# Kernel optimization log

Measured on AMD Instinct MI355X. Metric: run time of the kernel, lower is better.

## Reference

```python
import jax, jax.numpy as jnp
import numpy as np

EPS = 1e-5

def setup_inputs() -> dict:
    key = jax.random.key(0)
    ks = jax.random.split(key, 10)
    B, C, H, W = 4, 512, 56, 56
    n_heads = 8
    nq = H * W
    oq = (H // 2) * (W // 2)  # sr_ratio=2, k=3,s=2,p=1 -> halved spatial dims
    s = 0.02
    return {
        'x': jax.random.normal(ks[0], (B, C, H, W), jnp.float32),
        'attn_weights': jax.random.uniform(ks[1], (B, n_heads, nq, oq), jnp.float32),
        'q_w': jax.random.normal(ks[2], (C, C), jnp.float32) * s,
        'k_w': jax.random.normal(ks[3], (C, C), jnp.float32) * s,
        'v_w': jax.random.normal(ks[4], (C, C), jnp.float32) * s,
        'sr_w': jax.random.normal(ks[5], (C, 1, 3, 3), jnp.float32) * s,  # depthwise OIHW
        'sr_b': jnp.zeros((C,), jnp.float32),
        'ln_g': jnp.ones((C,), jnp.float32),
        'ln_b': jnp.zeros((C,), jnp.float32),
        'tc_w': jax.random.normal(ks[6], (n_heads, n_heads), jnp.float32) * 0.3,  # 1x1 conv over heads
        'tc_b': jnp.zeros((n_heads,), jnp.float32),
        'proj_w': jax.random.normal(ks[7], (C, C), jnp.float32) * s,
        'proj_b': jnp.zeros((C,), jnp.float32),
    }

def _layernorm(x, g, b):
    m = jnp.mean(x, axis=-1, keepdims=True)
    v = jnp.var(x, axis=-1, keepdims=True)
    return (x - m) * jax.lax.rsqrt(v + EPS) * g + b

def reference(x, attn_weights, q_w, k_w, v_w, sr_w, sr_b, ln_g, ln_b, tc_w, tc_b, proj_w, proj_b):
    B, C, H, W = x.shape
    n_heads = tc_w.shape[0]
    hd = C // n_heads
    scale = hd ** -0.5
    nq = H * W
    xf = x.reshape(B, C, nq).transpose(0, 2, 1)  # (B, nq, C)
    q = (xf @ q_w.T).reshape(B, nq, n_heads, hd).transpose(0, 2, 1, 3)  # (B, h, nq, hd)
    # spatial reduction: depthwise conv k=3, s=2, p=1 on NCHW, then LayerNorm
    xs = jax.lax.conv_general_dilated(
        x, sr_w, window_strides=(2, 2), padding=((1, 1), (1, 1)),
        feature_group_count=C, dimension_numbers=('NCHW', 'OIHW', 'NCHW'))
    xs = xs + sr_b[None, :, None, None]
    oq = xs.shape[2] * xs.shape[3]
    xs = xs.reshape(B, C, oq).transpose(0, 2, 1)  # (B, oq, C)
    xs = _layernorm(xs, ln_g, ln_b)
    k = (xs @ k_w.T).reshape(B, oq, n_heads, hd).transpose(0, 2, 3, 1)  # (B, h, hd, oq)
    v = (xs @ v_w.T).reshape(B, oq, n_heads, hd).transpose(0, 2, 1, 3)  # (B, h, oq, hd)
    attn = jnp.einsum('bhqd,bhdo->bhqo', q, k) * scale  # (B, h, nq, oq)
    # apply_transform: 1x1 conv mixing heads -> softmax -> InstanceNorm2d (no affine)
    attn = jnp.einsum('bhqo,gh->bgqo', attn, tc_w) + tc_b[None, :, None, None]
    attn = jax.nn.softmax(attn, axis=-1)
    m = jnp.mean(attn, axis=(2, 3), keepdims=True)
    var = jnp.var(attn, axis=(2, 3), keepdims=True)
    attn = (attn - m) * jax.lax.rsqrt(var + EPS)
    attn = attn_weights * attn
    out = jnp.einsum('bhqo,bhod->bhqd', attn, v)  # (B, h, nq, hd)
    out = out.transpose(0, 2, 1, 3).reshape(B, nq, C)
    out = out @ proj_w.T + proj_b
    return out.reshape(B, H, W, C).transpose(0, 3, 1, 2)
```

## Files before the change

### kernel.cpp

```cpp
#include <hip/hip_runtime.h>

typedef _Float16 half8 __attribute__((ext_vector_type(8)));
typedef _Float16 half4 __attribute__((ext_vector_type(4)));
typedef float fx4 __attribute__((ext_vector_type(4)));

#define MFMA16(a,b,c) __builtin_amdgcn_mfma_f32_16x16x32_f16(a,b,c,0,0,0)

#define BN 4
#define CC 512
#define HH 56
#define WW 56
#define NQ 3136
#define OQ 784
#define NH 8
#define HD 64
#define NSEG 7
#define BGN (BN * NH * NQ)

__device__ inline half8 h8z() {
    half8 v;
#pragma unroll
    for (int j = 0; j < 8; j++) v[j] = (_Float16)0.f;
    return v;
}

__global__ void cvt4_kernel(const float* __restrict__ a, const float* __restrict__ b,
                            const float* __restrict__ c, const float* __restrict__ d,
                            _Float16* __restrict__ o, float* __restrict__ S2) {
    if (blockIdx.x == 0 && blockIdx.y == 0 && threadIdx.x < 32) S2[threadIdx.x] = 0.f;
    int y = blockIdx.y;
    const float* s = (y == 0) ? a : (y == 1) ? b : (y == 2) ? c : d;
    int i = blockIdx.x * 256 + threadIdx.x;
    o[(size_t)y * 262144 + i] = (_Float16)s[i];
}

__global__ void xpose_kernel(const float* __restrict__ x, _Float16* __restrict__ xf) {
    __shared__ float t[32][33];
    int n0 = blockIdx.x * 32, c0 = blockIdx.y * 32, b = blockIdx.z;
    int tx = threadIdx.x, ty = threadIdx.y;
#pragma unroll
    for (int i = 0; i < 4; i++)
        t[ty + 8 * i][tx] = x[((size_t)(b * CC) + c0 + ty + 8 * i) * NQ + n0 + tx];
    __syncthreads();
#pragma unroll
    for (int i = 0; i < 4; i++)
        xf[((size_t)(b * NQ) + n0 + ty + 8 * i) * CC + c0 + tx] = (_Float16)t[tx][ty + 8 * i];
}

__global__ void dw_kernel(const float* __restrict__ x, const float* __restrict__ w,
                          const float* __restrict__ bias, float* __restrict__ xsc) {
    int cb = blockIdx.x, oy = blockIdx.y, b = blockIdx.z;
    int tx = threadIdx.x, ty = threadIdx.y;
    int c = cb * 16 + ty;
    float a = bias[c];
    const float* xp = x + ((size_t)(b * CC + c) * HH) * WW;
#pragma unroll
    for (int ky = 0; ky < 3; ky++) {
        int iy = 2 * oy - 1 + ky;
        if (iy < 0 || iy >= HH) continue;
#pragma unroll
        for (int kx = 0; kx < 3; kx++) {
            int ix = 2 * tx - 1 + kx;
            if (ix < 0 || ix >= WW) continue;
            a += xp[iy * WW + ix] * w[c * 9 + ky * 3 + kx];
        }
    }
    __shared__ float tile[28][17];
    tile[tx][ty] = a;
    __syncthreads();
    int lin = ty * 28 + tx;
    int oi = lin >> 4, ci = lin & 15;
    xsc[((size_t)(b * OQ) + oy * 28 + oi) * CC + cb * 16 + ci] = tile[oi][ci];
}

__global__ __launch_bounds__(256) void ln_kernel(const float* __restrict__ xsc,
        const float* __restrict__ g, const float* __restrict__ bb,
        _Float16* __restrict__ xs16) {
    int row = blockIdx.x;
    const float* rp = xsc + (size_t)row * CC;
    int t = threadIdx.x;
    float v0 = rp[t], v1 = rp[t + 256];
    float s = v0 + v1, ss = v0 * v0 + v1 * v1;
#pragma unroll
    for (int m = 1; m < 64; m <<= 1) {
        s += __shfl_xor(s, m, 64);
        ss += __shfl_xor(ss, m, 64);
    }
    __shared__ float red[8];
    int wv = t >> 6;
    if ((t & 63) == 0) { red[wv] = s; red[4 + wv] = ss; }
    __syncthreads();
    s = red[0] + red[1] + red[2] + red[3];
    ss = red[4] + red[5] + red[6] + red[7];
    float mean = s * (1.f / 512.f);
    float var = ss * (1.f / 512.f) - mean * mean;
    float rs = rsqrtf(var + 1e-5f);
    xs16[(size_t)row * CC + t] = (_Float16)((v0 - mean) * rs * g[t] + bb[t]);
    xs16[(size_t)row * CC + t + 256] = (_Float16)((v1 - mean) * rs * g[t + 256] + bb[t + 256]);
}

__global__ __launch_bounds__(256) void gemm_qkv(const _Float16* __restrict__ xf,
        const _Float16* __restrict__ xs, const _Float16* __restrict__ w4,
        _Float16* __restrict__ q16, _Float16* __restrict__ k16, _Float16* __restrict__ vT) {
    const int which = blockIdx.z;
    if (which && blockIdx.x >= 49) return;
    const _Float16* A = which ? xs : xf;
    const _Float16* Bw = w4 + (size_t)which * 262144;
    __shared__ _Float16 As[64 * 72];
    __shared__ _Float16 Bs[64 * 72];
    const int m0 = blockIdx.x * 64, n0 = blockIdx.y * 64;
    const int tid = threadIdx.x;
    const int lane = tid & 63, wv = tid >> 6;
    const int wm = (wv >> 1) * 32, wn = (wv & 1) * 32;
    const int l15 = lane & 15, quad = lane >> 4;
    fx4 acc[2][2];
#pragma unroll
    for (int i = 0; i < 2; i++)
#pragma unroll
        for (int j = 0; j < 2; j++) acc[i][j] = fx4{0.f, 0.f, 0.f, 0.f};
    for (int k0 = 0; k0 < 512; k0 += 64) {
        __syncthreads();
#pragma unroll
        for (int i = 0; i < 2; i++) {
            int id = tid + 256 * i;
            int r = id >> 3, kc = (id & 7) << 3;
            *(half8*)(As + r * 72 + kc) = *(const half8*)(A + (size_t)(m0 + r) * 512 + k0 + kc);
            *(half8*)(Bs + r * 72 + kc) = *(const half8*)(Bw + (size_t)(n0 + r) * 512 + k0 + kc);
        }
        __syncthreads();
#pragma unroll
        for (int ks = 0; ks < 2; ks++) {
            half8 af[2], bf[2];
#pragma unroll
            for (int s = 0; s < 2; s++) {
                af[s] = *(const half8*)(As + (wm + s * 16 + l15) * 72 + ks * 32 + quad * 8);
                bf[s] = *(const half8*)(Bs + (wn + s * 16 + l15) * 72 + ks * 32 + quad * 8);
            }
#pragma unroll
            for (int i = 0; i < 2; i++)
#pragma unroll
                for (int j = 0; j < 2; j++)
                    acc[i][j] = MFMA16(af[i], bf[j], acc[i][j]);
        }
    }
    if (which < 2) {
        _Float16* O = which ? k16 : q16;
#pragma unroll
        for (int i = 0; i < 2; i++)
#pragma unroll
            for (int j = 0; j < 2; j++) {
                int col = n0 + wn + j * 16 + l15;
#pragma unroll
                for (int e = 0; e < 4; e++) {
                    int row = m0 + wm + i * 16 + quad * 4 + e;
                    O[(size_t)row * 512 + col] = (_Float16)acc[i][j][e];
                }
            }
    } else {
#pragma unroll
        for (int i = 0; i < 2; i++) {
            int row = m0 + wm + i * 16 + quad * 4;
            int b = row / OQ;
            int o = row - b * OQ;
#pragma unroll
            for (int j = 0; j < 2; j++) {
                int c = n0 + wn + j * 16 + l15;
                half4 pk;
#pragma unroll
                for (int e = 0; e < 4; e++) pk[e] = (_Float16)acc[i][j][e];
                *(half4*)(vT + ((size_t)(b * NH + (c >> 6)) * HD + (c & 63)) * OQ + o) = pk;
            }
        }
    }
}

__global__ __launch_bounds__(256) void qk_mix(const _Float16* __restrict__ q16,
        const _Float16* __restrict__ k16, const float* __restrict__ tcw,
        const float* __restrict__ tcb, _Float16* __restrict__ L,
        float* __restrict__ Zpart, float* __restrict__ E2part) {
    __shared__ _Float16 kl[16 * 520];
    __shared__ float tcs[64];
    __shared__ float tbb[8];
    const int b = blockIdx.z, oseg = blockIdx.y, ob = oseg * 112;
    const int tid = threadIdx.x;
    const int wv = tid >> 6, lane = tid & 63, l15 = lane & 15, quad = lane >> 4;
    const int n0 = blockIdx.x * 64 + wv * 16;
    if (tid < 64) tcs[tid] = tcw[tid] * 0.125f;
    else if (tid < 72) tbb[tid - 64] = tcb[tid - 64];

    half8 aF[8][2];
    const _Float16* qrow = q16 + ((size_t)(b * NQ + n0 + l15)) * 512;
#pragma unroll
    for (int h = 0; h < 8; h++)
#pragma unroll
        for (int ks = 0; ks < 2; ks++)
            aF[h][ks] = *(const half8*)(qrow + h * 64 + ks * 32 + quad * 8);

    float z[8][4], s2[8][4];
#pragma unroll
    for (int g = 0; g < 8; g++)
#pragma unroll
        for (int e = 0; e < 4; e++) { z[g][e] = 0.f; s2[g][e] = 0.f; }

    for (int ot = 0; ot < 7; ot++) {
        int o0 = ob + ot * 16;
        __syncthreads();
        const _Float16* kb = k16 + ((size_t)(b * OQ + o0)) * 512;
#pragma unroll
        for (int i = 0; i < 4; i++) {
            int id = tid + 256 * i;
            int r = id >> 6, c = (id & 63) << 3;
            *(half8*)(kl + r * 520 + c) = *(const half8*)(kb + (size_t)r * 512 + c);
        }
        __syncthreads();
        fx4 s[8];
#pragma unroll
        for (int h = 0; h < 8; h++) {
            fx4 a = fx4{0.f, 0.f, 0.f, 0.f};
#pragma unroll
            for (int ks = 0; ks < 2; ks++) {
                half8 bF = *(const half8*)(kl + l15 * 520 + h * 64 + ks * 32 + quad * 8);
                a = MFMA16(aF[h][ks], bF, a);
            }
            s[h] = a;
        }
#pragma unroll
        for (int g = 0; g < 8; g++) {
            size_t tb = (((size_t)(b * 8 + g) * 196 + (n0 >> 4)) * 49 + (o0 >> 4)) * 256
                        + (l15 >> 3) * 128 + (l15 & 7);
#pragma unroll
            for (int e = 0; e < 4; e++) {
                float v = tbb[g];
#pragma unroll
                for (int h = 0; h < 8; h++) v += tcs[g * 8 + h] * s[h][e];
                _Float16 vh = (_Float16)v;
                float vr = (float)vh;
                float ex = __expf(vr);
                z[g][e] += ex;
                s2[g][e] += ex * ex;
                L[tb + (quad * 4 + e) * 8] = vh;
            }
        }
    }
#pragma unroll
    for (int m = 1; m < 16; m <<= 1) {
#pragma unroll
        for (int g = 0; g < 8; g++)
#pragma unroll
            for (int e = 0; e < 4; e++) {
                z[g][e] += __shfl_xor(z[g][e], m, 64);
                s2[g][e] += __shfl_xor(s2[g][e], m, 64);
            }
    }
    if (l15 < 8) {
        int g = l15;
        size_t base = (size_t)oseg * BGN + (size_t)(b * 8 + g) * NQ + n0 + quad * 4;
#pragma unroll
        for (int e = 0; e < 4; e++) {
            Zpart[base + e] = z[g][e];
            E2part[base + e] = s2[g][e];
        }
    }
}

__global__ __launch_bounds__(256) void zfin_kernel(const float* __restrict__ Zpart,
        const float* __restrict__ E2part, float* __restrict__ Zinv, float* __restrict__ S2) {
    int i = blockIdx.x * 256 + threadIdx.x;
    float z = 0.f, e2 = 0.f;
#pragma unroll
    for (int s = 0; s < NSEG; s++) {
        z += Zpart[(size_t)s * BGN + i];
        e2 += E2part[(size_t)s * BGN + i];
    }
    float zi = 1.f / z;
    Zinv[i] = zi;
    float r = e2 * zi * zi;
#pragma unroll
    for (int m = 1; m < 64; m <<= 1) r += __shfl_xor(r, m, 64);
    if ((threadIdx.x & 63) == 0) atomicAdd(&S2[i / NQ], r);
}

__global__ __launch_bounds__(256) void pv_kernel(const _Float16* __restrict__ Lt,
        const float* __restrict__ W, const _Float16* __restrict__ vT,
        const float* __restrict__ Zinv, const float* __restrict__ S2,
        _Float16* __restrict__ outp) {
    __shared__ float Ws[4][2][16 * 70];
    const int b = blockIdx.z, g = blockIdx.y;
    const int tid = threadIdx.x;
    const int wv = tid >> 6, lane = tid & 63, l15 = lane & 15, quad = lane >> 4;
    const int n0 = blockIdx.x * 64 + wv * 16;
    const int bg = b * 8 + g;
    const float mm = 1.f / (float)OQ;
    const float rv = rsqrtf(S2[bg] * (1.f / ((float)NQ * (float)OQ)) - mm * mm + 1e-5f);
    const float czr = Zinv[bg * NQ + n0 + l15] * rv;
    const float rm = rv * mm;
    const _Float16* Lb = Lt + (((size_t)bg * 196 + (n0 >> 4)) * 49) * 256 + lane * 8;
    const float* Wg = W + ((size_t)bg * NQ + n0 + (lane >> 4)) * OQ + (lane & 15) * 4;
    const float* Wrow = W + ((size_t)bg * NQ + n0 + l15) * OQ;
    const _Float16* vb = vT + (size_t)bg * HD * OQ + (size_t)l15 * OQ;
    float* WsW = &Ws[wv][0][0];
    const float* WsR = &Ws[wv][0][0] + l15 * 70 + quad * 8;

    fx4 wreg[4];
    half8 lA, lB, vA0, vA1, vA2, vA3, vB0, vB1, vB2, vB3;
    fx4 acc0 = fx4{0.f, 0.f, 0.f, 0.f};
    fx4 acc1 = fx4{0.f, 0.f, 0.f, 0.f};
    fx4 acc2 = fx4{0.f, 0.f, 0.f, 0.f};
    fx4 acc3 = fx4{0.f, 0.f, 0.f, 0.f};

#define LOADWG(g2)                                                           \
    {                                                                        \
        _Pragma("unroll") for (int i = 0; i < 4; i++)                        \
            wreg[i] = *(const fx4*)(Wg + (size_t)(4 * i) * OQ + (g2) * 64);  \
    }
#define DSWR(ph)                                                             \
    {                                                                        \
        _Pragma("unroll") for (int i = 0; i < 4; i++)                        \
            *(fx4*)(WsW + (ph) * (16 * 70) + ((lane >> 4) + 4 * i) * 70 +    \
                    (lane & 15) * 4) = wreg[i];                              \
    }
#define LOADL(c, d)                                                          \
    {                                                                        \
        if ((c) < 24 || lane < 32) d = *(const half8*)(Lb + (c) * 512);      \
        else d = h8z();                                                      \
    }
#define LOADV(c, d0, d1, d2, d3)                                             \
    {                                                                        \
        int kb = (c) * 32 + quad * 8;                                        \
        if (kb < OQ) {                                                       \
            d0 = *(const half8*)(vb + (size_t)(0 * 16) * OQ + kb);           \
            d1 = *(const half8*)(vb + (size_t)(1 * 16) * OQ + kb);           \
            d2 = *(const half8*)(vb + (size_t)(2 * 16) * OQ + kb);           \
            d3 = *(const half8*)(vb + (size_t)(3 * 16) * OQ + kb);           \
        } else { d0 = h8z(); d1 = h8z(); d2 = h8z(); d3 = h8z(); }           \
    }
#define COMPUTE_W(sL, wf0, wf1, s0, s1, s2, s3)                              \
    {                                                                        \
        half8 aH;                                                            \
        _Pragma("unroll") for (int j = 0; j < 8; j++) {                      \
            float e = __expf((float)sL[j]);                                  \
            float a = e * czr - rm;                                          \
            float wx = (j < 4) ? wf0[j] : wf1[j - 4];                        \
            aH[j] = (_Float16)(a * wx);                                      \
        }                                                                    \
        acc0 = MFMA16(aH, s0, acc0);                                         \
        acc1 = MFMA16(aH, s1, acc1);                                         \
        acc2 = MFMA16(aH, s2, acc2);                                         \
        acc3 = MFMA16(aH, s3, acc3);                                         \
    }

    LOADWG(0);
    LOADL(0, lA);
    LOADV(0, vA0, vA1, vA2, vA3);
    DSWR(0);
    LOADWG(1);

#pragma unroll 1
    for (int pi = 0; pi < 12; ++pi) {
        const int phC = pi & 1, phN = phC ^ 1;
        if (pi <= 10) DSWR(phN);
        if (pi <= 9) LOADWG(pi + 2);
        const int c0 = 2 * pi;
        LOADL(c0 + 1, lB);
        LOADV(c0 + 1, vB0, vB1, vB2, vB3);
        {
            const float* wr = WsR + phC * (16 * 70);
            fx4 wf0 = *(const fx4*)(wr);
            fx4 wf1 = *(const fx4*)(wr + 4);
            COMPUTE_W(lA, wf0, wf1, vA0, vA1, vA2, vA3);
        }
        LOADL(c0 + 2, lA);
        LOADV(c0 + 2, vA0, vA1, vA2, vA3);
        {
            const float* wr = WsR + phC * (16 * 70) + 32;
            fx4 wf0 = *(const fx4*)(wr);
            fx4 wf1 = *(const fx4*)(wr + 4);
            COMPUTE_W(lB, wf0, wf1, vB0, vB1, vB2, vB3);
        }
    }
    {
        fx4 wt0 = fx4{0.f, 0.f, 0.f, 0.f};
        fx4 wt1 = fx4{0.f, 0.f, 0.f, 0.f};
        int kb = 768 + quad * 8;
        if (kb < OQ) {
            wt0 = *(const fx4*)(Wrow + kb);
            wt1 = *(const fx4*)(Wrow + kb + 4);
        }
        COMPUTE_W(lA, wt0, wt1, vA0, vA1, vA2, vA3);
    }
#undef LOADWG
#undef DSWR
#undef LOADL
#undef LOADV
#undef COMPUTE_W

    fx4 acc[4] = {acc0, acc1, acc2, acc3};
#pragma unroll
    for (int ds = 0; ds < 4; ds++)
#pragma unroll
        for (int e = 0; e < 4; e++) {
            int n = n0 + quad * 4 + e;
            int c = g * 64 + ds * 16 + l15;
            outp[((size_t)b * NQ + n) * 512 + c] = (_Float16)acc[ds][e];
        }
}

__global__ __launch_bounds__(256) void gemm_proj(const _Float16* __restrict__ A,
        const _Float16* __restrict__ Ball, const float* __restrict__ bias,
        float* __restrict__ Oall) {
    __shared__ _Float16 As[64 * 72];
    __shared__ _Float16 Bs[64 * 72];
    const int b = blockIdx.z;
    const _Float16* Bm = Ball + (size_t)b * NQ * 512;
    float* O = Oall + (size_t)b * CC * NQ;
    const int m0 = blockIdx.x * 64, n0 = blockIdx.y * 64;
    const int tid = threadIdx.x;
    const int lane = tid & 63, wv = tid >> 6;
    const int wm = (wv >> 1) * 32, wn = (wv & 1) * 32;
    const int l15 = lane & 15, quad = lane >> 4;
    fx4 acc[2][2];
#pragma unroll
    for (int i = 0; i < 2; i++)
#pragma unroll
        for (int j = 0; j < 2; j++) acc[i][j] = fx4{0.f, 0.f, 0.f, 0.f};
    for (int k0 = 0; k0 < 512; k0 += 64) {
        __syncthreads();
#pragma unroll
        for (int i = 0; i < 2; i++) {
            int id = tid + 256 * i;
            int r = id >> 3, kc = (id & 7) << 3;
            *(half8*)(As + r * 72 + kc) = *(const half8*)(A + (size_t)(m0 + r) * 512 + k0 + kc);
            *(half8*)(Bs + r * 72 + kc) = *(const half8*)(Bm + (size_t)(n0 + r) * 512 + k0 + kc);
        }
        __syncthreads();
#pragma unroll
        for (int ks = 0; ks < 2; ks++) {
            half8 af[2], bf[2];
#pragma unroll
            for (int s = 0; s < 2; s++) {
                af[s] = *(const half8*)(As + (wm + s * 16 + l15) * 72 + ks * 32 + quad * 8);
                bf[s] = *(const half8*)(Bs + (wn + s * 16 + l15) * 72 + ks * 32 + quad * 8);
            }
#pragma unroll
            for (int i = 0; i < 2; i++)
#pragma unroll
                for (int j = 0; j < 2; j++)
                    acc[i][j] = MFMA16(af[i], bf[j], acc[i][j]);
        }
    }
#pragma unroll
    for (int i = 0; i < 2; i++)
#pragma unroll
        for (int j = 0; j < 2; j++) {
            int col = n0 + wn + j * 16 + l15;
#pragma unroll
            for (int e = 0; e < 4; e++) {
                int row = m0 + wm + i * 16 + quad * 4 + e;
                O[(size_t)row * NQ + col] = acc[i][j][e] + bias[row];
            }
        }
}

extern "C" void kernel_launch(void* const* d_in, const int* in_sizes, int n_in,
                              void* d_out, int out_size, void* d_ws, size_t ws_size,
                              hipStream_t stream) {
    const float* x = (const float*)d_in[0];
    const float* aw = (const float*)d_in[1];
    const float* q_w = (const float*)d_in[2];
    const float* k_w = (const float*)d_in[3];
    const float* v_w = (const float*)d_in[4];
    const float* sr_w = (const float*)d_in[5];
    const float* sr_b = (const float*)d_in[6];
    const float* ln_g = (const float*)d_in[7];
    const float* ln_b = (const float*)d_in[8];
    const float* tc_w = (const float*)d_in[9];
    const float* tc_b = (const float*)d_in[10];
    const float* p_w = (const float*)d_in[11];
    const float* p_b = (const float*)d_in[12];
    float* out = (float*)d_out;

    char* p = (char*)d_ws;
    auto take = [&](size_t bytes) -> char* {
        char* r = p;
        p += (bytes + 255) & ~(size_t)255;
        return r;
    };
    _Float16* qw16 = (_Float16*)take(512 * 512 * 2);
    _Float16* kw16 = (_Float16*)take(512 * 512 * 2);
    _Float16* vw16 = (_Float16*)take(512 * 512 * 2);
    _Float16* pw16 = (_Float16*)take(512 * 512 * 2);
    _Float16* xf16 = (_Float16*)take((size_t)BN * NQ * CC * 2);
    float* xsc = (float*)take((size_t)BN * OQ * CC * 4);
    _Float16* xs16 = (_Float16*)take((size_t)BN * OQ * CC * 2);
    _Float16* q16 = (_Float16*)take((size_t)BN * NQ * CC * 2);
    _Float16* k16 = (_Float16*)take((size_t)BN * OQ * CC * 2);
    _Float16* vT = (_Float16*)take((size_t)BN * OQ * CC * 2);
    _Float16* outp = (_Float16*)take((size_t)BN * NQ * CC * 2);
    float* Zpart = (float*)take((size_t)NSEG * BGN * 4);
    float* E2part = (float*)take((size_t)NSEG * BGN * 4);
    float* S2 = (float*)take(32 * 4);
    float* Zinv = (float*)take((size_t)BGN * 4);
    _Float16* L = (_Float16*)take((size_t)BN * NH * NQ * OQ * 2);

    cvt4_kernel<<<dim3(1024, 4), 256, 0, stream>>>(q_w, k_w, v_w, p_w, qw16, S2);
    xpose_kernel<<<dim3(98, 16, BN), dim3(32, 8), 0, stream>>>(x, xf16);
    dw_kernel<<<dim3(32, 28, BN), dim3(28, 16), 0, stream>>>(x, sr_w, sr_b, xsc);
    ln_kernel<<<BN * OQ, 256, 0, stream>>>(xsc, ln_g, ln_b, xs16);
    gemm_qkv<<<dim3(196, 8, 3), 256, 0, stream>>>(xf16, xs16, qw16, q16, k16, vT);
    qk_mix<<<dim3(49, 7, BN), 256, 0, stream>>>(q16, k16, tc_w, tc_b, L, Zpart, E2part);
    zfin_kernel<<<BGN / 256, 256, 0, stream>>>(Zpart, E2part, Zinv, S2);
    pv_kernel<<<dim3(49, 8, BN), 256, 0, stream>>>(L, aw, vT, Zinv, S2, outp);
    gemm_proj<<<dim3(8, 49, BN), 256, 0, stream>>>(pw16, outp, p_b, out);
}
```

Before: 706.5 us.

## Double-buffer LDS staging via direct global-to-LDS loads with XOR swizzle

The QKV GEMM, the QK/head-mix kernel and the projection GEMM now stage tiles into LDS with global_load_lds 16-byte direct loads instead of register round-trips. Each uses two LDS buffers so the next tile is prefetched while the current one is multiplied, which also drops one barrier per iteration. Padded rows are replaced by an XOR swizzle of 8-element groups to avoid bank conflicts. LDS use doubles, and correctness relies on the compiler waiting for the LDS DMA before the barriers.

```diff
diff --git a/kernel.cpp b/kernel.cpp
--- a/kernel.cpp
+++ b/kernel.cpp
@@ -22,6 +22,12 @@
 #pragma unroll
     for (int j = 0; j < 8; j++) v[j] = (_Float16)0.f;
     return v;
+}
+
+__device__ __forceinline__ void glds16(const void* g, void* l) {
+    __builtin_amdgcn_global_load_lds(
+        (__attribute__((address_space(1))) const unsigned int*)g,
+        (__attribute__((address_space(3))) unsigned int*)l, 16, 0, 0);
 }
 
 __global__ void cvt4_kernel(const float* __restrict__ a, const float* __restrict__ b,
@@ -106,8 +112,8 @@
     if (which && blockIdx.x >= 49) return;
     const _Float16* A = which ? xs : xf;
     const _Float16* Bw = w4 + (size_t)which * 262144;
-    __shared__ _Float16 As[64 * 72];
-    __shared__ _Float16 Bs[64 * 72];
+    __shared__ _Float16 As[2][64 * 64];
+    __shared__ _Float16 Bs[2][64 * 64];
     const int m0 = blockIdx.x * 64, n0 = blockIdx.y * 64;
     const int tid = threadIdx.x;
     const int lane = tid & 63, wv = tid >> 6;
@@ -118,23 +124,34 @@
     for (int i = 0; i < 2; i++)
 #pragma unroll
         for (int j = 0; j < 2; j++) acc[i][j] = fx4{0.f, 0.f, 0.f, 0.f};
-    for (int k0 = 0; k0 < 512; k0 += 64) {
-        __syncthreads();
-#pragma unroll
-        for (int i = 0; i < 2; i++) {
-            int id = tid + 256 * i;
-            int r = id >> 3, kc = (id & 7) << 3;
-            *(half8*)(As + r * 72 + kc) = *(const half8*)(A + (size_t)(m0 + r) * 512 + k0 + kc);
-            *(half8*)(Bs + r * 72 + kc) = *(const half8*)(Bw + (size_t)(n0 + r) * 512 + k0 + kc);
-        }
-        __syncthreads();
+
+#define STAGEG(bf, kk)                                                       \
+    {                                                                        \
+        _Pragma("unroll") for (int i = 0; i < 2; i++) {                      \
+            int id = tid + 256 * i;                                          \
+            int r = id >> 3, gg = id & 7;                                    \
+            int gs = gg ^ (r & 7);                                           \
+            glds16(A + (size_t)(m0 + r) * 512 + (kk) + gs * 8,               \
+                   &As[bf][(id & ~63) * 8]);                                 \
+            glds16(Bw + (size_t)(n0 + r) * 512 + (kk) + gs * 8,              \
+                   &Bs[bf][(id & ~63) * 8]);                                 \
+        }                                                                    \
+    }
+
+    STAGEG(0, 0);
+    __syncthreads();
+    for (int kt = 0; kt < 8; kt++) {
+        const int cur = kt & 1;
+        if (kt < 7) STAGEG(cur ^ 1, (kt + 1) * 64);
 #pragma unroll
         for (int ks = 0; ks < 2; ks++) {
             half8 af[2], bf[2];
 #pragma unroll
             for (int s = 0; s < 2; s++) {
-                af[s] = *(const half8*)(As + (wm + s * 16 + l15) * 72 + ks * 32 + quad * 8);
-                bf[s] = *(const half8*)(Bs + (wn + s * 16 + l15) * 72 + ks * 32 + quad * 8);
+                int ra = wm + s * 16 + l15;
+                int rb = wn + s * 16 + l15;
+                af[s] = *(const half8*)(&As[cur][ra * 64 + ((ks * 4 + quad) ^ (ra & 7)) * 8]);
+                bf[s] = *(const half8*)(&Bs[cur][rb * 64 + ((ks * 4 + quad) ^ (rb & 7)) * 8]);
             }
 #pragma unroll
             for (int i = 0; i < 2; i++)
@@ -142,7 +159,10 @@
                 for (int j = 0; j < 2; j++)
                     acc[i][j] = MFMA16(af[i], bf[j], acc[i][j]);
         }
-    }
+        __syncthreads();
+    }
+#undef STAGEG
+
     if (which < 2) {
         _Float16* O = which ? k16 : q16;
 #pragma unroll
@@ -178,7 +198,7 @@
         const _Float16* __restrict__ k16, const float* __restrict__ tcw,
         const float* __restrict__ tcb, _Float16* __restrict__ L,
         float* __restrict__ Zpart, float* __restrict__ E2part) {
-    __shared__ _Float16 kl[16 * 520];
+    __shared__ _Float16 kl[2][16 * 512];
     __shared__ float tcs[64];
     __shared__ float tbb[8];
     const int b = blockIdx.z, oseg = blockIdx.y, ob = oseg * 112;
@@ -202,24 +222,33 @@
 #pragma unroll
         for (int e = 0; e < 4; e++) { z[g][e] = 0.f; s2[g][e] = 0.f; }
 
+#define STAGEK(bf, oo)                                                       \
+    {                                                                        \
+        const _Float16* kbp = k16 + ((size_t)(b * OQ + (oo))) * 512;         \
+        _Pragma("unroll") for (int i = 0; i < 4; i++) {                      \
+            int id = tid + 256 * i;                                          \
+            int r = id >> 6, g16 = id & 63;                                  \
+            int gs = (g16 & 56) | ((g16 & 7) ^ (r & 7));                     \
+            glds16(kbp + (size_t)r * 512 + gs * 8, &kl[bf][(id & ~63) * 8]); \
+        }                                                                    \
+    }
+
+    STAGEK(0, ob);
+    __syncthreads();
+
     for (int ot = 0; ot < 7; ot++) {
+        const int cur = ot & 1;
+        if (ot < 6) STAGEK(cur ^ 1, ob + (ot + 1) * 16);
         int o0 = ob + ot * 16;
-        __syncthreads();
-        const _Float16* kb = k16 + ((size_t)(b * OQ + o0)) * 512;
-#pragma unroll
-        for (int i = 0; i < 4; i++) {
-            int id = tid + 256 * i;
-            int r = id >> 6, c = (id & 63) << 3;
-            *(half8*)(kl + r * 520 + c) = *(const half8*)(kb + (size_t)r * 512 + c);
-        }
-        __syncthreads();
         fx4 s[8];
 #pragma unroll
         for (int h = 0; h < 8; h++) {
             fx4 a = fx4{0.f, 0.f, 0.f, 0.f};
 #pragma unroll
             for (int ks = 0; ks < 2; ks++) {
-                half8 bF = *(const half8*)(kl + l15 * 520 + h * 64 + ks * 32 + quad * 8);
+                int colg = h * 8 + ks * 4 + quad;
+                int rg = (colg & 56) | ((colg & 7) ^ (l15 & 7));
+                half8 bF = *(const half8*)(&kl[cur][l15 * 512 + rg * 8]);
                 a = MFMA16(aF[h][ks], bF, a);
             }
             s[h] = a;
@@ -241,7 +270,10 @@
                 L[tb + (quad * 4 + e) * 8] = vh;
             }
         }
-    }
+        __syncthreads();
+    }
+#undef STAGEK
+
 #pragma unroll
     for (int m = 1; m < 16; m <<= 1) {
 #pragma unroll
@@ -408,8 +440,8 @@
 __global__ __launch_bounds__(256) void gemm_proj(const _Float16* __restrict__ A,
         const _Float16* __restrict__ Ball, const float* __restrict__ bias,
         float* __restrict__ Oall) {
-    __shared__ _Float16 As[64 * 72];
-    __shared__ _Float16 Bs[64 * 72];
+    __shared__ _Float16 As[2][64 * 64];
+    __shared__ _Float16 Bs[2][64 * 64];
     const int b = blockIdx.z;
     const _Float16* Bm = Ball + (size_t)b * NQ * 512;
     float* O = Oall + (size_t)b * CC * NQ;
@@ -423,23 +455,34 @@
     for (int i = 0; i < 2; i++)
 #pragma unroll
         for (int j = 0; j < 2; j++) acc[i][j] = fx4{0.f, 0.f, 0.f, 0.f};
-    for (int k0 = 0; k0 < 512; k0 += 64) {
-        __syncthreads();
-#pragma unroll
-        for (int i = 0; i < 2; i++) {
-            int id = tid + 256 * i;
-            int r = id >> 3, kc = (id & 7) << 3;
-            *(half8*)(As + r * 72 + kc) = *(const half8*)(A + (size_t)(m0 + r) * 512 + k0 + kc);
-            *(half8*)(Bs + r * 72 + kc) = *(const half8*)(Bm + (size_t)(n0 + r) * 512 + k0 + kc);
-        }
-        __syncthreads();
+
+#define STAGEP(bf, kk)                                                       \
+    {                                                                        \
+        _Pragma("unroll") for (int i = 0; i < 2; i++) {                      \
+            int id = tid + 256 * i;                                          \
+            int r = id >> 3, gg = id & 7;                                    \
+            int gs = gg ^ (r & 7);                                           \
+            glds16(A + (size_t)(m0 + r) * 512 + (kk) + gs * 8,               \
+                   &As[bf][(id & ~63) * 8]);                                 \
+            glds16(Bm + (size_t)(n0 + r) * 512 + (kk) + gs * 8,              \
+                   &Bs[bf][(id & ~63) * 8]);                                 \
+        }                                                                    \
+    }
+
+    STAGEP(0, 0);
+    __syncthreads();
+    for (int kt = 0; kt < 8; kt++) {
+        const int cur = kt & 1;
+        if (kt < 7) STAGEP(cur ^ 1, (kt + 1) * 64);
 #pragma unroll
         for (int ks = 0; ks < 2; ks++) {
             half8 af[2], bf[2];
 #pragma unroll
             for (int s = 0; s < 2; s++) {
-                af[s] = *(const half8*)(As + (wm + s * 16 + l15) * 72 + ks * 32 + quad * 8);
-                bf[s] = *(const half8*)(Bs + (wn + s * 16 + l15) * 72 + ks * 32 + quad * 8);
+                int ra = wm + s * 16 + l15;
+                int rb = wn + s * 16 + l15;
+                af[s] = *(const half8*)(&As[cur][ra * 64 + ((ks * 4 + quad) ^ (ra & 7)) * 8]);
+                bf[s] = *(const half8*)(&Bs[cur][rb * 64 + ((ks * 4 + quad) ^ (rb & 7)) * 8]);
             }
 #pragma unroll
             for (int i = 0; i < 2; i++)
@@ -447,7 +490,10 @@
                 for (int j = 0; j < 2; j++)
                     acc[i][j] = MFMA16(af[i], bf[j], acc[i][j]);
         }
-    }
+        __syncthreads();
+    }
+#undef STAGEP
+
 #pragma unroll
     for (int i = 0; i < 2; i++)
 #pragma unroll
```

Result: no change. 706.9 us (+0.1%).
